# Kernel optimization log

Measured on AMD Instinct MI355X. Metric: run time of the kernel, lower is better.

Reference implementation:

```python
import jax, jax.numpy as jnp
import numpy as np

L = 262144
C = 64           # in_channels == out_channels (required by zeros_like scatter)
NUM_MODES = 64

def setup_inputs() -> dict:
    key = jax.random.key(0)
    k1, k2, k3, k4 = jax.random.split(key, 4)
    u = jax.random.normal(k1, (L, C), dtype=jnp.float32)
    y = jax.random.uniform(k2, (1, 1), dtype=jnp.float32)
    scale = 1.0 / (C * C)
    K = scale * jax.random.normal(k3, (2, C, C, NUM_MODES), dtype=jnp.float32)
    # glorot_normal for square (C, C)
    W = jax.random.normal(k4, (C, C), dtype=jnp.float32) * jnp.sqrt(2.0 / (C + C))
    return {"u": u, "y": y, "K": K, "W": W}

def reference(u, y, K, W):
    num_modes = K.shape[-1]
    out_ch = W.shape[0]
    # conditioner: spectral (global) branch
    u_hat = jnp.fft.rfft(u, axis=0)                      # (L//2+1, C) complex64
    Kc = K[0] + 1j * K[1]                                # (C, C, num_modes)
    z_modes = jnp.einsum('xi,iox->xo', u_hat[:num_modes], Kc)  # (num_modes, C)
    z_global = jnp.zeros_like(u_hat).at[:num_modes, :].set(z_modes)
    # conditioner: local branch (gather one spatial row, apply W)
    length = u.shape[0]
    idx = jnp.int32(y * length)[0][0]
    z_local = jnp.dot(W, u[idx, :out_ch])                # (C,)
    # basefield: inverse transform + local shift
    n = 2 * (z_global.shape[0] - 1)                      # == L
    s = jnp.fft.irfft(z_global, n=n, axis=0)             # (L, C)
    return s + z_local
```

## Files before the change

### kernel.cpp

```cpp
#include <hip/hip_runtime.h>

#define LN 262144
#define LMASK 262143
#define NCH 64
#define INV_L (1.0f/262144.0f)
#define BSTR 38
#define ISTR 138
#define XSTR 66

typedef short short8 __attribute__((ext_vector_type(8)));
typedef float f32x4 __attribute__((ext_vector_type(4)));

union s8i4 { int4 i; short8 s; };

static __device__ __forceinline__ unsigned pkbf(float lo, float hi) {
    union { float f; unsigned u; } a, b; a.f = lo; b.f = hi;
    return __builtin_amdgcn_perm(b.u, a.u, 0x07060302u);
}
static __device__ __forceinline__ short8 pk8(const float* v) {
    s8i4 cv;
    cv.i = make_int4(pkbf(v[0], v[1]), pkbf(v[2], v[3]),
                     pkbf(v[4], v[5]), pkbf(v[6], v[7]));
    return cv.s;
}
static __device__ __forceinline__ unsigned short f2bf_t(float x) {
    union { float f; unsigned u; } v; v.f = x;
    return (unsigned short)(v.u >> 16);
}
static __device__ __forceinline__ float fsin01(float rev) {
    float r; asm("v_sin_f32 %0, %1" : "=v"(r) : "v"(rev)); return r;
}
static __device__ __forceinline__ float fcos01(float rev) {
    float r; asm("v_cos_f32 %0, %1" : "=v"(r) : "v"(rev)); return r;
}

__global__ __launch_bounds__(256) void fno_fwd(const float* __restrict__ u,
                                               float* __restrict__ part, int nb) {
    __shared__ __align__(16) unsigned short Bt[2][64 * BSTR];
    const int tid = threadIdx.x;
    const int lane = tid & 63;
    const int w = tid >> 6;
    const int chunk = LN / nb;
    const int ksteps = chunk >> 5;
    const int n0 = blockIdx.x * chunk;

    const int kkst = tid >> 3;
    const int gst = tid & 7;

    const int l15 = lane & 15;
    const int hk = lane >> 4;
    const int m = w * 16 + l15;

    float cR[8], nsR[8];
    #pragma unroll
    for (int j = 0; j < 8; ++j) {
        int ph = (m * (n0 + hk * 8 + j)) & LMASK;
        cR[j] = fcos01((float)ph * INV_L);
        nsR[j] = -fsin01((float)ph * INV_L);
    }
    float cD, sD;
    {
        int ph = (m * 32) & LMASK;
        cD = fcos01((float)ph * INV_L);
        sD = fsin01((float)ph * INV_L);
    }

    f32x4 accC[4], accS[4];
    #pragma unroll
    for (int t = 0; t < 4; ++t) { accC[t] = (f32x4){0,0,0,0}; accS[t] = (f32x4){0,0,0,0}; }

    const float* __restrict__ ub = u + (size_t)(n0 + kkst) * NCH + gst * 8;
    const size_t tstep = 32 * NCH;

    float4 a0 = *(const float4*)(ub);
    float4 a1 = *(const float4*)(ub + 4);
    float4 b0 = *(const float4*)(ub + tstep);
    float4 b1 = *(const float4*)(ub + tstep + 4);
    {
        float uv[8] = {a0.x, a0.y, a0.z, a0.w, a1.x, a1.y, a1.z, a1.w};
        #pragma unroll
        for (int q = 0; q < 8; ++q)
            Bt[0][(gst * 8 + q) * BSTR + kkst] = f2bf_t(uv[q]);
    }
    a0 = b0; a1 = b1;
    b0 = *(const float4*)(ub + 2 * tstep);
    b1 = *(const float4*)(ub + 2 * tstep + 4);

    for (int t = 0; t < ksteps; ++t) {
        __syncthreads();
        if (t + 1 < ksteps) {
            float uv[8] = {a0.x, a0.y, a0.z, a0.w, a1.x, a1.y, a1.z, a1.w};
            unsigned short* bt = Bt[(t + 1) & 1];
            #pragma unroll
            for (int q = 0; q < 8; ++q)
                bt[(gst * 8 + q) * BSTR + kkst] = f2bf_t(uv[q]);
        }
        a0 = b0; a1 = b1;
        if (t + 3 < ksteps) {
            const float* pn = ub + (size_t)(t + 3) * tstep;
            b0 = *(const float4*)(pn);
            b1 = *(const float4*)(pn + 4);
        }
        const short8 aC = pk8(cR);
        const short8 aS = pk8(nsR);
        #pragma unroll
        for (int j = 0; j < 8; ++j) {
            float c2 = cR[j] * cD + nsR[j] * sD;
            nsR[j] = nsR[j] * cD - cR[j] * sD;
            cR[j] = c2;
        }
        const unsigned short* bt = Bt[t & 1];
        #pragma unroll
        for (int tn = 0; tn < 4; ++tn) {
            const short8 bf = *(const short8*)&bt[(tn * 16 + l15) * BSTR + hk * 8];
            accC[tn] = __builtin_amdgcn_mfma_f32_16x16x32_bf16(aC, bf, accC[tn], 0, 0, 0);
            accS[tn] = __builtin_amdgcn_mfma_f32_16x16x32_bf16(aS, bf, accS[tn], 0, 0, 0);
        }
    }
    float* baseR = part + (size_t)blockIdx.x * 8192;
    #pragma unroll
    for (int tn = 0; tn < 4; ++tn) {
        #pragma unroll
        for (int r = 0; r < 4; ++r) {
            int k = w * 16 + hk * 4 + r;
            int i = tn * 16 + l15;
            baseR[k * 64 + i] = accC[tn][r];
            baseR[4096 + k * 64 + i] = accS[tn][r];
        }
    }
}

__global__ __launch_bounds__(512) void fno_redcoef(const float* __restrict__ part, int nb,
                                                   const float* __restrict__ Kt,
                                                   const float* __restrict__ W,
                                                   const float* __restrict__ u,
                                                   const float* __restrict__ y,
                                                   float* __restrict__ coef) {
    const int k = blockIdx.x;
    const int t = threadIdx.x;
    const int j = t & 31;
    const int h = t >> 5;

    const float* __restrict__ pb =
        part + (size_t)k * 64 + (j & 15) * 4 + ((j >> 4) ? 4096 : 0);
    float4 s4 = make_float4(0.f, 0.f, 0.f, 0.f);
    #pragma unroll 4
    for (int b = h; b < nb; b += 16) {
        float4 v = *(const float4*)&pb[(size_t)b * 8192];
        s4.x += v.x; s4.y += v.y; s4.z += v.z; s4.w += v.w;
    }
    __shared__ float4 red4[16][32];
    __shared__ float uh[128];
    red4[h][j] = s4;
    __syncthreads();
    if (t < 32) {
        float4 acc = red4[0][t];
        #pragma unroll
        for (int hh = 1; hh < 16; ++hh) {
            float4 v = red4[hh][t];
            acc.x += v.x; acc.y += v.y; acc.z += v.z; acc.w += v.w;
        }
        const int base = (t >> 4) * 64 + (t & 15) * 4;
        uh[base + 0] = acc.x; uh[base + 1] = acc.y;
        uh[base + 2] = acc.z; uh[base + 3] = acc.w;
    }
    __syncthreads();

    if (t < 64) {
        const int o = t;
        float zr = 0.f, zi = 0.f;
        #pragma unroll 8
        for (int ii = 0; ii < 64; ++ii) {
            float k0v = Kt[(size_t)(ii * 64 + o) * 64 + k];
            float k1v = Kt[262144 + (size_t)(ii * 64 + o) * 64 + k];
            zr = fmaf(uh[ii], k0v, fmaf(-uh[64 + ii], k1v, zr));
            zi = fmaf(uh[ii], k1v, fmaf(uh[64 + ii], k0v, zi));
        }
        if (k == 0) {
            const int idx = (int)(y[0] * (float)LN);
            float zl = 0.f;
            for (int ii = 0; ii < 64; ++ii)
                zl = fmaf(W[o * 64 + ii], u[(size_t)idx * 64 + ii], zl);
            coef[o] = zr * INV_L;
            coef[4096 + o] = 0.f;
            coef[8192 + o] = zl;
        } else {
            coef[k * 64 + o] = 2.f * zr * INV_L;
            coef[4096 + k * 64 + o] = -2.f * zi * INV_L;
        }
    }
}

__global__ __launch_bounds__(256) void fno_inv(const float* __restrict__ coef,
                                               float* __restrict__ out) {
    __shared__ __align__(16) unsigned short Bs[64 * ISTR];
    __shared__ float zloc[64];
    __shared__ float xpose[4][16 * XSTR];
    const int tid = threadIdx.x;
    const int lane = tid & 63;
    const int w = tid >> 6;

    for (int e = tid; e < 4096; e += 256) {
        int mm = e >> 6, ch = e & 63;
        Bs[ch * ISTR + mm] = f2bf_t(coef[e]);
        Bs[ch * ISTR + 64 + mm] = f2bf_t(coef[4096 + e]);
    }
    if (tid < 64) zloc[tid] = coef[8192 + tid];
    __syncthreads();

    const int l15 = lane & 15;
    const int hk = lane >> 4;
    const int rl = lane >> 4;
    const int cq = lane & 15;
    float4 zv = *(const float4*)&zloc[cq * 4];

    for (int p = 0; p < 4; ++p) {
        const int nbase = blockIdx.x * 256 + (p * 4 + w) * 16;
        const int row = nbase + l15;
        float cstp = fcos01((float)row * INV_L);
        float sstp = fsin01((float)row * INV_L);

        short8 aF[4];
        #pragma unroll
        for (int h = 0; h < 2; ++h) {
            const int m0 = h * 32 + hk * 8;
            const int ph = (row * m0) & LMASK;
            float c = fcos01((float)ph * INV_L);
            float s = fsin01((float)ph * INV_L);
            float cv[8], sv[8];
            #pragma unroll
            for (int jj = 0; jj < 8; ++jj) {
                cv[jj] = c; sv[jj] = s;
                float c2 = c * cstp - s * sstp;
                s = fmaf(s, cstp, c * sstp);
                c = c2;
            }
            aF[h] = pk8(cv);
            aF[2 + h] = pk8(sv);
        }

        f32x4 acc[4];
        #pragma unroll
        for (int tn = 0; tn < 4; ++tn) acc[tn] = (f32x4){0,0,0,0};
        #pragma unroll
        for (int ks = 0; ks < 4; ++ks) {
            #pragma unroll
            for (int tn = 0; tn < 4; ++tn) {
                const short8 bf = *(const short8*)&Bs[(tn * 16 + l15) * ISTR + ks * 32 + hk * 8];
                acc[tn] = __builtin_amdgcn_mfma_f32_16x16x32_bf16(aF[ks], bf, acc[tn], 0, 0, 0);
            }
        }
        #pragma unroll
        for (int tn = 0; tn < 4; ++tn)
            #pragma unroll
            for (int r = 0; r < 4; ++r)
                xpose[w][(hk * 4 + r) * XSTR + tn * 16 + l15] = acc[tn][r];
        asm volatile("s_waitcnt lgkmcnt(0)" ::: "memory");
        #pragma unroll
        for (int rg = 0; rg < 4; ++rg) {
            const int rowl = rg * 4 + rl;
            float4 v = *(const float4*)&xpose[w][rowl * XSTR + cq * 4];
            v.x += zv.x; v.y += zv.y; v.z += zv.z; v.w += zv.w;
            *(float4*)(out + (size_t)(nbase + rowl) * NCH + cq * 4) = v;
        }
    }
}

extern "C" void kernel_launch(void* const* d_in, const int* in_sizes, int n_in,
                              void* d_out, int out_size, void* d_ws, size_t ws_size,
                              hipStream_t stream) {
    const float* u = (const float*)d_in[0];
    const float* y = (const float*)d_in[1];
    const float* K = (const float*)d_in[2];
    const float* W = (const float*)d_in[3];
    float* out = (float*)d_out;
    float* ws = (float*)d_ws;

    int nb = 512;
    while (nb > 64 && ((size_t)(nb * 8192 + 8256) * 4) > ws_size) nb >>= 1;

    float* part = ws;
    float* coef = ws + (size_t)nb * 8192;

    fno_fwd<<<nb, 256, 0, stream>>>(u, part, nb);
    fno_redcoef<<<64, 512, 0, stream>>>(part, nb, K, W, u, y, coef);
    fno_inv<<<1024, 256, 0, stream>>>(coef, out);
}
```

Before: 60.00 us.

## Store partial DFT sums as bf16 and split reduction from coefficient kernel

The forward kernel now writes its per-block partial spectral sums as bf16 instead of fp32, which halves the partial buffer traffic. The combined reduce-and-coefficient kernel is split in two. A 256-block reduction kernel gives wider parallelism over the partial sums, and a small 64-block kernel applies the K mixing and the local branch. This adds an extra launch and more bf16 rounding error in the accumulated spectrum.

```diff
diff --git a/kernel.cpp b/kernel.cpp
--- a/kernel.cpp
+++ b/kernel.cpp
@@ -27,6 +27,10 @@
     union { float f; unsigned u; } v; v.f = x;
     return (unsigned short)(v.u >> 16);
 }
+static __device__ __forceinline__ float bf2f(unsigned short b) {
+    union { unsigned u; float f; } v; v.u = ((unsigned)b) << 16;
+    return v.f;
+}
 static __device__ __forceinline__ float fsin01(float rev) {
     float r; asm("v_sin_f32 %0, %1" : "=v"(r) : "v"(rev)); return r;
 }
@@ -35,7 +39,7 @@
 }
 
 __global__ __launch_bounds__(256) void fno_fwd(const float* __restrict__ u,
-                                               float* __restrict__ part, int nb) {
+                                               unsigned short* __restrict__ part, int nb) {
     __shared__ __align__(16) unsigned short Bt[2][64 * BSTR];
     const int tid = threadIdx.x;
     const int lane = tid & 63;
@@ -117,77 +121,79 @@
             accS[tn] = __builtin_amdgcn_mfma_f32_16x16x32_bf16(aS, bf, accS[tn], 0, 0, 0);
         }
     }
-    float* baseR = part + (size_t)blockIdx.x * 8192;
+    unsigned short* baseR = part + (size_t)blockIdx.x * 8192;
     #pragma unroll
     for (int tn = 0; tn < 4; ++tn) {
         #pragma unroll
         for (int r = 0; r < 4; ++r) {
             int k = w * 16 + hk * 4 + r;
             int i = tn * 16 + l15;
-            baseR[k * 64 + i] = accC[tn][r];
-            baseR[4096 + k * 64 + i] = accS[tn][r];
-        }
-    }
-}
-
-__global__ __launch_bounds__(512) void fno_redcoef(const float* __restrict__ part, int nb,
-                                                   const float* __restrict__ Kt,
-                                                   const float* __restrict__ W,
-                                                   const float* __restrict__ u,
-                                                   const float* __restrict__ y,
-                                                   float* __restrict__ coef) {
-    const int k = blockIdx.x;
+            baseR[k * 64 + i] = f2bf_t(accC[tn][r]);
+            baseR[4096 + k * 64 + i] = f2bf_t(accS[tn][r]);
+        }
+    }
+}
+
+__global__ __launch_bounds__(256) void fno_red(const unsigned short* __restrict__ part, int nb,
+                                               float* __restrict__ uhat) {
     const int t = threadIdx.x;
-    const int j = t & 31;
-    const int h = t >> 5;
-
-    const float* __restrict__ pb =
-        part + (size_t)k * 64 + (j & 15) * 4 + ((j >> 4) ? 4096 : 0);
-    float4 s4 = make_float4(0.f, 0.f, 0.f, 0.f);
-    #pragma unroll 4
-    for (int b = h; b < nb; b += 16) {
-        float4 v = *(const float4*)&pb[(size_t)b * 8192];
-        s4.x += v.x; s4.y += v.y; s4.z += v.z; s4.w += v.w;
-    }
-    __shared__ float4 red4[16][32];
-    __shared__ float uh[128];
-    red4[h][j] = s4;
+    const int sp = t & 3;
+    const int bi = t >> 2;
+    const int g0 = blockIdx.x * 32;
+
+    float acc[8] = {0,0,0,0,0,0,0,0};
+    for (int b = bi; b < nb; b += 64) {
+        short8 v = *(const short8*)&part[(size_t)b * 8192 + g0 + sp * 8];
+        #pragma unroll
+        for (int e = 0; e < 8; ++e)
+            acc[e] += bf2f((unsigned short)v[e]);
+    }
+    __shared__ float red[64][36];
+    #pragma unroll
+    for (int e = 0; e < 8; ++e)
+        red[bi][sp * 8 + e] = acc[e];
     __syncthreads();
     if (t < 32) {
-        float4 acc = red4[0][t];
-        #pragma unroll
-        for (int hh = 1; hh < 16; ++hh) {
-            float4 v = red4[hh][t];
-            acc.x += v.x; acc.y += v.y; acc.z += v.z; acc.w += v.w;
-        }
-        const int base = (t >> 4) * 64 + (t & 15) * 4;
-        uh[base + 0] = acc.x; uh[base + 1] = acc.y;
-        uh[base + 2] = acc.z; uh[base + 3] = acc.w;
-    }
+        float s = 0.f;
+        #pragma unroll 16
+        for (int b2 = 0; b2 < 64; ++b2)
+            s += red[b2][t];
+        uhat[g0 + t] = s;
+    }
+}
+
+__global__ __launch_bounds__(64) void fno_coef(const float* __restrict__ uhat,
+                                               const float* __restrict__ Kt,
+                                               const float* __restrict__ W,
+                                               const float* __restrict__ u,
+                                               const float* __restrict__ y,
+                                               float* __restrict__ coef) {
+    const int k = blockIdx.x;
+    const int o = threadIdx.x;
+    __shared__ float re[64], im[64];
+    re[o] = uhat[k * 64 + o];
+    im[o] = uhat[4096 + k * 64 + o];
     __syncthreads();
-
-    if (t < 64) {
-        const int o = t;
-        float zr = 0.f, zi = 0.f;
+    float zr = 0.f, zi = 0.f;
+    #pragma unroll 8
+    for (int ii = 0; ii < 64; ++ii) {
+        float k0v = Kt[(size_t)(ii * 64 + o) * 64 + k];
+        float k1v = Kt[262144 + (size_t)(ii * 64 + o) * 64 + k];
+        zr = fmaf(re[ii], k0v, fmaf(-im[ii], k1v, zr));
+        zi = fmaf(re[ii], k1v, fmaf(im[ii], k0v, zi));
+    }
+    if (k == 0) {
+        const int idx = (int)(y[0] * (float)LN);
+        float zl = 0.f;
         #pragma unroll 8
-        for (int ii = 0; ii < 64; ++ii) {
-            float k0v = Kt[(size_t)(ii * 64 + o) * 64 + k];
-            float k1v = Kt[262144 + (size_t)(ii * 64 + o) * 64 + k];
-            zr = fmaf(uh[ii], k0v, fmaf(-uh[64 + ii], k1v, zr));
-            zi = fmaf(uh[ii], k1v, fmaf(uh[64 + ii], k0v, zi));
-        }
-        if (k == 0) {
-            const int idx = (int)(y[0] * (float)LN);
-            float zl = 0.f;
-            for (int ii = 0; ii < 64; ++ii)
-                zl = fmaf(W[o * 64 + ii], u[(size_t)idx * 64 + ii], zl);
-            coef[o] = zr * INV_L;
-            coef[4096 + o] = 0.f;
-            coef[8192 + o] = zl;
-        } else {
-            coef[k * 64 + o] = 2.f * zr * INV_L;
-            coef[4096 + k * 64 + o] = -2.f * zi * INV_L;
-        }
+        for (int ii = 0; ii < 64; ++ii)
+            zl = fmaf(W[o * 64 + ii], u[(size_t)idx * 64 + ii], zl);
+        coef[o] = zr * INV_L;
+        coef[4096 + o] = 0.f;
+        coef[8192 + o] = zl;
+    } else {
+        coef[k * 64 + o] = 2.f * zr * INV_L;
+        coef[4096 + k * 64 + o] = -2.f * zi * INV_L;
     }
 }
 
@@ -274,15 +280,16 @@
     const float* K = (const float*)d_in[2];
     const float* W = (const float*)d_in[3];
     float* out = (float*)d_out;
-    float* ws = (float*)d_ws;
 
     int nb = 512;
-    while (nb > 64 && ((size_t)(nb * 8192 + 8256) * 4) > ws_size) nb >>= 1;
-
-    float* part = ws;
-    float* coef = ws + (size_t)nb * 8192;
+    while (nb > 64 && ((size_t)nb * 8192 * 2 + (size_t)(8192 + 8256) * 4) > ws_size) nb >>= 1;
+
+    unsigned short* part = (unsigned short*)d_ws;
+    float* uhat = (float*)((char*)d_ws + (size_t)nb * 8192 * 2);
+    float* coef = uhat + 8192;
 
     fno_fwd<<<nb, 256, 0, stream>>>(u, part, nb);
-    fno_redcoef<<<64, 512, 0, stream>>>(part, nb, K, W, u, y, coef);
+    fno_red<<<256, 256, 0, stream>>>(part, nb, uhat);
+    fno_coef<<<64, 64, 0, stream>>>(uhat, K, W, u, y, coef);
     fno_inv<<<1024, 256, 0, stream>>>(coef, out);
 }
```

New measurement: 60.87 us. No clear change (+1.4%).
